# Kernel optimization log

Hardware: AMD Instinct MI355X
Metric: run time of the kernel (lower is better)

## Reference

```python
import jax, jax.numpy as jnp
import numpy as np
import math

NUM_HEADS = 16


def _alibi_slopes(num_heads: int):
    # geometric sequence for power-of-2 head counts (paper's scheme)
    def slopes_pow2(n):
        start = 2.0 ** (-(2.0 ** (-(math.log2(n) - 3))))
        return [start * (start ** i) for i in range(n)]
    if math.log2(num_heads).is_integer():
        return slopes_pow2(num_heads)
    c = 2 ** math.floor(math.log2(num_heads))
    extra = slopes_pow2(2 * c)[0::2][: num_heads - c]
    return slopes_pow2(c) + extra


def setup_inputs() -> dict:
    key = jax.random.key(0)
    kq, kk, kv = jax.random.split(key, 3)
    B, H, S, D = 2, NUM_HEADS, 2048, 64
    q = jax.random.normal(kq, (B, H, S, D), dtype=jnp.float32)
    k = jax.random.normal(kk, (B, H, S, D), dtype=jnp.float32)
    v = jax.random.normal(kv, (B, H, S, D), dtype=jnp.float32)
    return {"q": q, "k": k, "v": v}


def reference(q, k, v):
    B, H, Sq, D = q.shape
    Sk = k.shape[2]
    slopes = jnp.asarray(_alibi_slopes(H), dtype=jnp.float32)  # [H]
    pos = jnp.arange(Sk)
    # abs relative positions (symmetric, non-causal) as in the source
    rel = jnp.abs(pos[None, :] - pos[:, None]).astype(jnp.float32)  # [Sk, Sk]
    alibi = -slopes[:, None, None] * rel[None, :Sq, :]  # [H, Sq, Sk]
    scores = jnp.einsum("bhqd,bhkd->bhqk", q, k) / math.sqrt(D)
    scores = scores + alibi[None]
    probs = jax.nn.softmax(scores, axis=-1)
    return jnp.einsum("bhqk,bhkd->bhqd", probs, v)
```

## Files before the change

kernel.cpp:

```cpp
#include <hip/hip_runtime.h>
#include <hip/hip_bf16.h>
#include <math.h>

typedef __bf16 bf16;
typedef __attribute__((ext_vector_type(8))) bf16 bf16x8;
typedef __attribute__((ext_vector_type(2))) bf16 bf16x2;
typedef __attribute__((ext_vector_type(16))) float f32x16;
typedef __attribute__((ext_vector_type(4))) unsigned int uint4v;

#define SQ 2048
#define DH 64
#define NH 16
#define QBLK 128
#define KVT 64
#define NKVT (SQ / KVT)
#define LOG2E 1.44269504088896340736f

#define BUFSZ 16384
#define LDSV  8192

__device__ __forceinline__ int swz(int row, int colbyte) {
    return row * 128 + (colbyte ^ ((row & 7) << 4));
}

__device__ __forceinline__ float fast_exp2(float x) {
#if __has_builtin(__builtin_amdgcn_exp2f)
    return __builtin_amdgcn_exp2f(x);
#else
    return exp2f(x);
#endif
}

__device__ __forceinline__ unsigned pkbf16(float a, float b) {
    union { bf16x2 h; unsigned u; } x;
    x.h = (bf16x2){(bf16)a, (bf16)b};
    return x.u;
}

#if __has_builtin(__builtin_amdgcn_permlane32_swap)
__device__ __forceinline__ void plswap(unsigned &a, unsigned &b) {
    typedef __attribute__((ext_vector_type(2))) unsigned int uint2v;
    uint2v r = __builtin_amdgcn_permlane32_swap(a, b, false, false);
    a = r[0]; b = r[1];
}
#else
__device__ __forceinline__ void plswap(unsigned &a, unsigned &b) {
    asm volatile("v_permlane32_swap_b32 %0, %1" : "+v"(a), "+v"(b));
}
#endif

#if __has_builtin(__builtin_amdgcn_global_load_lds)
#define HAVE_GLL 1
__device__ __forceinline__ void async_copy16(const bf16* g, char* l) {
    __builtin_amdgcn_global_load_lds(
        (const __attribute__((address_space(1))) unsigned int*)g,
        (__attribute__((address_space(3))) unsigned int*)l, 16, 0, 0);
}
#else
#define HAVE_GLL 0
#endif

union FragU { uint4v u; bf16x8 b; };

__global__ __launch_bounds__(256)
void alibi_prep_kernel(const float* __restrict__ K, const float* __restrict__ V,
                       bf16* __restrict__ Kb, bf16* __restrict__ Vtb) {
    __shared__ bf16 lt[64][72];
    const int t  = threadIdx.x;
    const int s0 = blockIdx.x * 64;
    const int bh = blockIdx.y;
    if (blockIdx.z == 0) {
        const float* src = K + (size_t)bh * SQ * DH + (size_t)s0 * DH;
        bf16* dst = Kb + (size_t)bh * SQ * DH + (size_t)s0 * DH;
#pragma unroll
        for (int i = 0; i < 2; ++i) {
            int idx = t + 256 * i;
            int row = idx >> 3, c8 = idx & 7;
            const float* p = src + row * DH + c8 * 8;
            float4 a = *(const float4*)p, b = *(const float4*)(p + 4);
            bf16x8 pk = {(bf16)a.x,(bf16)a.y,(bf16)a.z,(bf16)a.w,
                         (bf16)b.x,(bf16)b.y,(bf16)b.z,(bf16)b.w};
            *(bf16x8*)(dst + row * DH + c8 * 8) = pk;
        }
    } else {
        const float* src = V + (size_t)bh * SQ * DH + (size_t)s0 * DH;
#pragma unroll
        for (int i = 0; i < 2; ++i) {
            int idx = t + 256 * i;
            int row = idx >> 3, c8 = idx & 7;
            const float* p = src + row * DH + c8 * 8;
            float4 a = *(const float4*)p, b = *(const float4*)(p + 4);
            bf16 e[8] = {(bf16)a.x,(bf16)a.y,(bf16)a.z,(bf16)a.w,
                         (bf16)b.x,(bf16)b.y,(bf16)b.z,(bf16)b.w};
#pragma unroll
            for (int j = 0; j < 8; ++j) lt[c8 * 8 + j][row] = e[j];
        }
        __syncthreads();
        bf16* dst = Vtb + (size_t)bh * DH * SQ;
#pragma unroll
        for (int i = 0; i < 2; ++i) {
            int idx = t + 256 * i;
            int d = idx >> 3, c8 = idx & 7;
            *(bf16x8*)(dst + (size_t)d * SQ + s0 + c8 * 8) = *(const bf16x8*)&lt[d][c8 * 8];
        }
    }
}

__global__ __launch_bounds__(256)
void alibi_attn_kernel(const float* __restrict__ Q, const bf16* __restrict__ Kb,
                       const bf16* __restrict__ Vtb, float* __restrict__ Out) {
    __shared__ __align__(16) char lds[3 * BUFSZ];
    const int tid  = threadIdx.x;
    const int lane = tid & 63;
    const int wave = tid >> 6;
    const int r32  = lane & 31;
    const int hi   = lane >> 5;
    const int l8   = lane >> 3;

    const int b   = blockIdx.x;
    const int r   = (b < 256) ? b : 767 - b;
    const int h   = 15 - (r >> 5);
    const int sub = r & 31;
    const int bh  = (sub >> 4) * NH + h;
    const int q0  = (sub & 15) * QBLK;

    const float slope2  = exp2f(-0.5f * (float)(h + 1)) * LOG2E;
    const float SLOPE2N = -slope2;
    const float QSCALE  = 0.125f * LOG2E;

    const int D = (int)(24.0f / slope2);
    const int a0 = q0 - D;
    const int tmin = (a0 <= 0) ? 0 : (a0 >> 6);
    const int tmax = min(NKVT - 1, (q0 + QBLK - 1 + D) >> 6);

    const size_t base = (size_t)bh * SQ * DH;
    const float* Qp = Q + base;
    const bf16*  Kp = Kb + base;
    const bf16*  Vp = Vtb + base;
    float*       Op = Out + base;

    const int qrow = q0 + wave * 32 + r32;
    bf16x8 qfrag[4];
#pragma unroll
    for (int dstep = 0; dstep < 4; ++dstep) {
        const float* sq = Qp + (size_t)qrow * DH + dstep * 16 + hi * 8;
        float4 a = *(const float4*)sq, bb = *(const float4*)(sq + 4);
        qfrag[dstep] = (bf16x8){(bf16)(a.x*QSCALE),(bf16)(a.y*QSCALE),
                                (bf16)(a.z*QSCALE),(bf16)(a.w*QSCALE),
                                (bf16)(bb.x*QSCALE),(bf16)(bb.y*QSCALE),
                                (bf16)(bb.z*QSCALE),(bf16)(bb.w*QSCALE)};
    }

    f32x16 oacc[2];
#pragma unroll
    for (int d = 0; d < 2; ++d)
#pragma unroll
        for (int rr = 0; rr < 16; ++rr) oacc[d][rr] = 0.f;
    float ps0 = 0.f, ps1 = 0.f, ps2 = 0.f, ps3 = 0.f;
    const float qh = (float)(qrow - 4 * hi);

    const int cswz = ((lane & 7) << 4) ^ ((l8 & 7) << 4);

    auto STAGE = [&](int bufi, int kvtile) {
        char* lb = lds + bufi * BUFSZ;
        const int kv0 = kvtile * KVT;
#pragma unroll
        for (int i = 0; i < 2; ++i) {
            const int chunk = wave * 2 + i;
            const int row = chunk * 8 + l8;
            const bf16* gK = Kp + (size_t)(kv0 + row) * DH + (cswz >> 1);
            const bf16* gV = Vp + (size_t)row * SQ + kv0 + (cswz >> 1);
#if HAVE_GLL
            async_copy16(gK, lb + chunk * 1024);
            async_copy16(gV, lb + LDSV + chunk * 1024);
#else
            *(bf16x8*)(lb + chunk * 1024 + lane * 16) = *(const bf16x8*)gK;
            *(bf16x8*)(lb + LDSV + chunk * 1024 + lane * 16) = *(const bf16x8*)gV;
#endif
        }
    };

    STAGE(0, tmin);
    STAGE(1, tmin + 1);
    asm volatile("s_waitcnt vmcnt(4)" ::: "memory");
    __builtin_amdgcn_s_barrier();
    __builtin_amdgcn_sched_barrier(0);

    int cb = 0, sb = 2;

    for (int t = tmin; t <= tmax; ++t) {
        const int kv0 = t * KVT;
        const char* lb = lds + cb * BUFSZ;

        f32x16 sacc[2];
        __builtin_amdgcn_s_setprio(1);
#pragma unroll
        for (int blk = 0; blk < 2; ++blk) {
            f32x16 acc;
#pragma unroll
            for (int rr = 0; rr < 16; ++rr) acc[rr] = 0.f;
#pragma unroll
            for (int dstep = 0; dstep < 4; ++dstep) {
                bf16x8 kf = *(const bf16x8*)(lb + swz(blk * 32 + r32, dstep * 32 + hi * 16));
                acc = __builtin_amdgcn_mfma_f32_32x32x16_bf16(kf, qfrag[dstep], acc, 0, 0, 0);
            }
            sacc[blk] = acc;
        }
        __builtin_amdgcn_s_setprio(0);

        STAGE(sb, min(t + 2, tmax));

        const float gq = qh - (float)kv0;
        float p[32];
#pragma unroll
        for (int blk = 0; blk < 2; ++blk)
#pragma unroll
            for (int reg = 0; reg < 16; ++reg) {
                const int krel = (reg & 3) + 8 * (reg >> 2) + 32 * blk;
                float d = gq - (float)krel;
                float s2 = fmaf(SLOPE2N, fabsf(d), sacc[blk][reg]);
                float e = fast_exp2(s2);
                p[blk * 16 + reg] = e;
                if ((reg & 3) == 0) ps0 += e;
                else if ((reg & 3) == 1) ps1 += e;
                else if ((reg & 3) == 2) ps2 += e;
                else ps3 += e;
            }

        __builtin_amdgcn_s_setprio(1);
#pragma unroll
        for (int kstep = 0; kstep < 4; ++kstep) {
            const int b16 = (kstep >> 1) * 16;
            const int R = (kstep & 1) * 8;
            unsigned w0 = pkbf16(p[b16 + R + 0], p[b16 + R + 1]);
            unsigned w1 = pkbf16(p[b16 + R + 2], p[b16 + R + 3]);
            unsigned w2 = pkbf16(p[b16 + R + 4], p[b16 + R + 5]);
            unsigned w3 = pkbf16(p[b16 + R + 6], p[b16 + R + 7]);
            plswap(w0, w2);
            plswap(w1, w3);
            FragU pf; pf.u = (uint4v){w0, w1, w2, w3};
#pragma unroll
            for (int dblk = 0; dblk < 2; ++dblk) {
                bf16x8 vf = *(const bf16x8*)(lb + LDSV + swz(dblk * 32 + r32, kstep * 32 + hi * 16));
                oacc[dblk] = __builtin_amdgcn_mfma_f32_32x32x16_bf16(vf, pf.b, oacc[dblk], 0, 0, 0);
            }
        }
        __builtin_amdgcn_s_setprio(0);

        asm volatile("s_waitcnt vmcnt(4)" ::: "memory");
        __builtin_amdgcn_s_barrier();
        __builtin_amdgcn_sched_barrier(0);

        cb = (cb == 2) ? 0 : cb + 1;
        sb = (sb == 2) ? 0 : sb + 1;
    }

    float psum = (ps0 + ps1) + (ps2 + ps3);
    psum += __shfl_xor(psum, 32);
    const float inv = 1.f / psum;
#pragma unroll
    for (int dblk = 0; dblk < 2; ++dblk)
#pragma unroll
        for (int g2 = 0; g2 < 4; ++g2) {
            float4 o = {oacc[dblk][4*g2+0] * inv, oacc[dblk][4*g2+1] * inv,
                        oacc[dblk][4*g2+2] * inv, oacc[dblk][4*g2+3] * inv};
            *(float4*)(Op + (size_t)qrow * DH + dblk * 32 + g2 * 8 + hi * 4) = o;
        }
}

extern "C" void kernel_launch(void* const* d_in, const int* in_sizes, int n_in,
                              void* d_out, int out_size, void* d_ws, size_t ws_size,
                              hipStream_t stream) {
    const float* q = (const float*)d_in[0];
    const float* k = (const float*)d_in[1];
    const float* v = (const float*)d_in[2];
    float* out = (float*)d_out;
    const int BH = in_sizes[0] / (SQ * DH);
    bf16* Kb  = (bf16*)d_ws;
    bf16* Vtb = (bf16*)((char*)d_ws + (size_t)BH * SQ * DH * sizeof(bf16));
    alibi_prep_kernel<<<dim3(SQ / 64, BH, 2), dim3(256), 0, stream>>>(k, v, Kb, Vtb);
    alibi_attn_kernel<<<dim3(512), dim3(256), 0, stream>>>(q, Kb, Vtb, out);
}
```

Before: 54.02 us.

## Split KV tiles across wave pairs with smaller Q blocks and LDS reduction

Q block size is halved to 64 rows, which doubles the grid to 1024 blocks. Inside each block the two wave pairs handle alternate KV tiles for the same 64 query rows, and their partial outputs and row sums are combined through LDS at the end. The triple-buffered async prefetch is replaced by a load, wait-all, compute loop, and launch bounds now ask for 4 blocks per CU. The aim is better occupancy and load balance across the alibi-banded work, at the cost of losing overlap between loads and compute and adding an epilogue reduction.

```diff
diff --git a/kernel.cpp b/kernel.cpp
--- a/kernel.cpp
+++ b/kernel.cpp
@@ -11,13 +11,14 @@
 #define SQ 2048
 #define DH 64
 #define NH 16
-#define QBLK 128
+#define QBLK 64
 #define KVT 64
 #define NKVT (SQ / KVT)
 #define LOG2E 1.44269504088896340736f
 
-#define BUFSZ 16384
+#define PBUF  16384
 #define LDSV  8192
+#define LDS_BYTES 32768
 
 __device__ __forceinline__ int swz(int row, int colbyte) {
     return row * 128 + (colbyte ^ ((row & 7) << 4));
@@ -106,23 +107,31 @@
     }
 }
 
-__global__ __launch_bounds__(256)
+__global__ __launch_bounds__(256, 4)
 void alibi_attn_kernel(const float* __restrict__ Q, const bf16* __restrict__ Kb,
                        const bf16* __restrict__ Vtb, float* __restrict__ Out) {
-    __shared__ __align__(16) char lds[3 * BUFSZ];
-    const int tid  = threadIdx.x;
-    const int lane = tid & 63;
-    const int wave = tid >> 6;
-    const int r32  = lane & 31;
-    const int hi   = lane >> 5;
-    const int l8   = lane >> 3;
-
-    const int b   = blockIdx.x;
-    const int r   = (b < 256) ? b : 767 - b;
-    const int h   = 15 - (r >> 5);
-    const int sub = r & 31;
-    const int bh  = (sub >> 4) * NH + h;
-    const int q0  = (sub & 15) * QBLK;
+    __shared__ __align__(16) char lds[LDS_BYTES];
+    const int tid   = threadIdx.x;
+    const int lane  = tid & 63;
+    const int wave  = tid >> 6;
+    const int par   = wave >> 1;
+    const int kind  = wave & 1;
+    const int qhalf = wave & 1;
+    const int r32   = lane & 31;
+    const int hi    = lane >> 5;
+    const int l8    = lane >> 3;
+
+    const int b  = blockIdx.x;
+    const int qd = b >> 8, i = b & 255;
+    int r;
+    if      (qd == 0) r = i;
+    else if (qd == 1) r = 511 - i;
+    else if (qd == 2) r = 512 + i;
+    else              r = 1023 - i;
+    const int h   = 15 - (r >> 6);
+    const int sub = r & 63;
+    const int bh  = (sub >> 5) * NH + h;
+    const int q0  = (sub & 31) * QBLK;
 
     const float slope2  = exp2f(-0.5f * (float)(h + 1)) * LOG2E;
     const float SLOPE2N = -slope2;
@@ -132,6 +141,7 @@
     const int a0 = q0 - D;
     const int tmin = (a0 <= 0) ? 0 : (a0 >> 6);
     const int tmax = min(NKVT - 1, (q0 + QBLK - 1 + D) >> 6);
+    const int nsteps = ((tmax - tmin + 1) + 1) >> 1;
 
     const size_t base = (size_t)bh * SQ * DH;
     const float* Qp = Q + base;
@@ -139,7 +149,7 @@
     const bf16*  Vp = Vtb + base;
     float*       Op = Out + base;
 
-    const int qrow = q0 + wave * 32 + r32;
+    const int qrow = q0 + qhalf * 32 + r32;
     bf16x8 qfrag[4];
 #pragma unroll
     for (int dstep = 0; dstep < 4; ++dstep) {
@@ -159,113 +169,142 @@
     float ps0 = 0.f, ps1 = 0.f, ps2 = 0.f, ps3 = 0.f;
     const float qh = (float)(qrow - 4 * hi);
 
-    const int cswz = ((lane & 7) << 4) ^ ((l8 & 7) << 4);
-
-    auto STAGE = [&](int bufi, int kvtile) {
-        char* lb = lds + bufi * BUFSZ;
-        const int kv0 = kvtile * KVT;
-#pragma unroll
-        for (int i = 0; i < 2; ++i) {
-            const int chunk = wave * 2 + i;
-            const int row = chunk * 8 + l8;
-            const bf16* gK = Kp + (size_t)(kv0 + row) * DH + (cswz >> 1);
-            const bf16* gV = Vp + (size_t)row * SQ + kv0 + (cswz >> 1);
+    const int cswz = ((lane & 7) << 4) ^ (l8 << 4);
+    char* const sbuf = lds + par * PBUF + kind * LDSV;
+    const char* const cbuf = lds + par * PBUF;
+
+    for (int s = 0; s < nsteps; ++s) {
+        const int tc = tmin + 2 * s + par;
+        const int ts = min(tc, tmax);
+
+        {
+            const int kv0s = ts * KVT;
+            if (kind == 0) {
+#pragma unroll
+                for (int c = 0; c < 8; ++c) {
+                    const int row = c * 8 + l8;
+                    const bf16* gK = Kp + (size_t)(kv0s + row) * DH + (cswz >> 1);
 #if HAVE_GLL
-            async_copy16(gK, lb + chunk * 1024);
-            async_copy16(gV, lb + LDSV + chunk * 1024);
-#else
-            *(bf16x8*)(lb + chunk * 1024 + lane * 16) = *(const bf16x8*)gK;
-            *(bf16x8*)(lb + LDSV + chunk * 1024 + lane * 16) = *(const bf16x8*)gV;
-#endif
-        }
-    };
-
-    STAGE(0, tmin);
-    STAGE(1, tmin + 1);
-    asm volatile("s_waitcnt vmcnt(4)" ::: "memory");
-    __builtin_amdgcn_s_barrier();
-    __builtin_amdgcn_sched_barrier(0);
-
-    int cb = 0, sb = 2;
-
-    for (int t = tmin; t <= tmax; ++t) {
-        const int kv0 = t * KVT;
-        const char* lb = lds + cb * BUFSZ;
-
-        f32x16 sacc[2];
-        __builtin_amdgcn_s_setprio(1);
-#pragma unroll
-        for (int blk = 0; blk < 2; ++blk) {
-            f32x16 acc;
-#pragma unroll
-            for (int rr = 0; rr < 16; ++rr) acc[rr] = 0.f;
-#pragma unroll
-            for (int dstep = 0; dstep < 4; ++dstep) {
-                bf16x8 kf = *(const bf16x8*)(lb + swz(blk * 32 + r32, dstep * 32 + hi * 16));
-                acc = __builtin_amdgcn_mfma_f32_32x32x16_bf16(kf, qfrag[dstep], acc, 0, 0, 0);
-            }
-            sacc[blk] = acc;
-        }
-        __builtin_amdgcn_s_setprio(0);
-
-        STAGE(sb, min(t + 2, tmax));
-
-        const float gq = qh - (float)kv0;
-        float p[32];
-#pragma unroll
-        for (int blk = 0; blk < 2; ++blk)
-#pragma unroll
-            for (int reg = 0; reg < 16; ++reg) {
-                const int krel = (reg & 3) + 8 * (reg >> 2) + 32 * blk;
-                float d = gq - (float)krel;
-                float s2 = fmaf(SLOPE2N, fabsf(d), sacc[blk][reg]);
-                float e = fast_exp2(s2);
-                p[blk * 16 + reg] = e;
-                if ((reg & 3) == 0) ps0 += e;
-                else if ((reg & 3) == 1) ps1 += e;
-                else if ((reg & 3) == 2) ps2 += e;
-                else ps3 += e;
-            }
-
-        __builtin_amdgcn_s_setprio(1);
-#pragma unroll
-        for (int kstep = 0; kstep < 4; ++kstep) {
-            const int b16 = (kstep >> 1) * 16;
-            const int R = (kstep & 1) * 8;
-            unsigned w0 = pkbf16(p[b16 + R + 0], p[b16 + R + 1]);
-            unsigned w1 = pkbf16(p[b16 + R + 2], p[b16 + R + 3]);
-            unsigned w2 = pkbf16(p[b16 + R + 4], p[b16 + R + 5]);
-            unsigned w3 = pkbf16(p[b16 + R + 6], p[b16 + R + 7]);
-            plswap(w0, w2);
-            plswap(w1, w3);
-            FragU pf; pf.u = (uint4v){w0, w1, w2, w3};
-#pragma unroll
-            for (int dblk = 0; dblk < 2; ++dblk) {
-                bf16x8 vf = *(const bf16x8*)(lb + LDSV + swz(dblk * 32 + r32, kstep * 32 + hi * 16));
-                oacc[dblk] = __builtin_amdgcn_mfma_f32_32x32x16_bf16(vf, pf.b, oacc[dblk], 0, 0, 0);
-            }
-        }
-        __builtin_amdgcn_s_setprio(0);
-
-        asm volatile("s_waitcnt vmcnt(4)" ::: "memory");
+                    async_copy16(gK, sbuf + c * 1024);
+#else
+                    *(bf16x8*)(sbuf + c * 1024 + lane * 16) = *(const bf16x8*)gK;
+#endif
+                }
+            } else {
+#pragma unroll
+                for (int c = 0; c < 8; ++c) {
+                    const int row = c * 8 + l8;
+                    const bf16* gV = Vp + (size_t)row * SQ + kv0s + (cswz >> 1);
+#if HAVE_GLL
+                    async_copy16(gV, sbuf + c * 1024);
+#else
+                    *(bf16x8*)(sbuf + c * 1024 + lane * 16) = *(const bf16x8*)gV;
+#endif
+                }
+            }
+        }
+        asm volatile("s_waitcnt vmcnt(0)" ::: "memory");
         __builtin_amdgcn_s_barrier();
         __builtin_amdgcn_sched_barrier(0);
 
-        cb = (cb == 2) ? 0 : cb + 1;
-        sb = (sb == 2) ? 0 : sb + 1;
+        if (tc <= tmax) {
+            const int kv0 = tc * KVT;
+
+            f32x16 sacc[2];
+            __builtin_amdgcn_s_setprio(1);
+#pragma unroll
+            for (int blk = 0; blk < 2; ++blk) {
+                f32x16 acc;
+#pragma unroll
+                for (int rr = 0; rr < 16; ++rr) acc[rr] = 0.f;
+#pragma unroll
+                for (int dstep = 0; dstep < 4; ++dstep) {
+                    bf16x8 kf = *(const bf16x8*)(cbuf + swz(blk * 32 + r32, dstep * 32 + hi * 16));
+                    acc = __builtin_amdgcn_mfma_f32_32x32x16_bf16(kf, qfrag[dstep], acc, 0, 0, 0);
+                }
+                sacc[blk] = acc;
+            }
+            __builtin_amdgcn_s_setprio(0);
+
+            const float gq = qh - (float)kv0;
+            float p[32];
+#pragma unroll
+            for (int blk = 0; blk < 2; ++blk)
+#pragma unroll
+                for (int reg = 0; reg < 16; ++reg) {
+                    const int krel = (reg & 3) + 8 * (reg >> 2) + 32 * blk;
+                    float d = gq - (float)krel;
+                    float s2 = fmaf(SLOPE2N, fabsf(d), sacc[blk][reg]);
+                    float e = fast_exp2(s2);
+                    p[blk * 16 + reg] = e;
+                    if ((reg & 3) == 0) ps0 += e;
+                    else if ((reg & 3) == 1) ps1 += e;
+                    else if ((reg & 3) == 2) ps2 += e;
+                    else ps3 += e;
+                }
+
+            __builtin_amdgcn_s_setprio(1);
+#pragma unroll
+            for (int kstep = 0; kstep < 4; ++kstep) {
+                const int b16 = (kstep >> 1) * 16;
+                const int R = (kstep & 1) * 8;
+                unsigned w0 = pkbf16(p[b16 + R + 0], p[b16 + R + 1]);
+                unsigned w1 = pkbf16(p[b16 + R + 2], p[b16 + R + 3]);
+                unsigned w2 = pkbf16(p[b16 + R + 4], p[b16 + R + 5]);
+                unsigned w3 = pkbf16(p[b16 + R + 6], p[b16 + R + 7]);
+                plswap(w0, w2);
+                plswap(w1, w3);
+                FragU pf; pf.u = (uint4v){w0, w1, w2, w3};
+#pragma unroll
+                for (int dblk = 0; dblk < 2; ++dblk) {
+                    bf16x8 vf = *(const bf16x8*)(cbuf + LDSV + swz(dblk * 32 + r32, kstep * 32 + hi * 16));
+                    oacc[dblk] = __builtin_amdgcn_mfma_f32_32x32x16_bf16(vf, pf.b, oacc[dblk], 0, 0, 0);
+                }
+            }
+            __builtin_amdgcn_s_setprio(0);
+        }
+        __builtin_amdgcn_s_barrier();
+        __builtin_amdgcn_sched_barrier(0);
     }
 
     float psum = (ps0 + ps1) + (ps2 + ps3);
     psum += __shfl_xor(psum, 32);
-    const float inv = 1.f / psum;
-#pragma unroll
-    for (int dblk = 0; dblk < 2; ++dblk)
-#pragma unroll
-        for (int g2 = 0; g2 < 4; ++g2) {
-            float4 o = {oacc[dblk][4*g2+0] * inv, oacc[dblk][4*g2+1] * inv,
-                        oacc[dblk][4*g2+2] * inv, oacc[dblk][4*g2+3] * inv};
-            *(float4*)(Op + (size_t)qrow * DH + dblk * 32 + g2 * 8 + hi * 4) = o;
-        }
+
+    __syncthreads();
+    float* ep = (float*)lds + qhalf * (64 * 36);
+    float* slot = ep + lane * 36;
+    if (par == 1) {
+#pragma unroll
+        for (int dblk = 0; dblk < 2; ++dblk)
+#pragma unroll
+            for (int g2 = 0; g2 < 4; ++g2)
+                *(float4*)(slot + dblk * 16 + g2 * 4) =
+                    (float4){oacc[dblk][4*g2+0], oacc[dblk][4*g2+1],
+                             oacc[dblk][4*g2+2], oacc[dblk][4*g2+3]};
+        slot[32] = psum;
+    }
+    __syncthreads();
+    if (par == 0) {
+#pragma unroll
+        for (int dblk = 0; dblk < 2; ++dblk)
+#pragma unroll
+            for (int g2 = 0; g2 < 4; ++g2) {
+                float4 o = *(const float4*)(slot + dblk * 16 + g2 * 4);
+                oacc[dblk][4*g2+0] += o.x; oacc[dblk][4*g2+1] += o.y;
+                oacc[dblk][4*g2+2] += o.z; oacc[dblk][4*g2+3] += o.w;
+            }
+        psum += slot[32];
+
+        const float inv = 1.f / psum;
+#pragma unroll
+        for (int dblk = 0; dblk < 2; ++dblk)
+#pragma unroll
+            for (int g2 = 0; g2 < 4; ++g2) {
+                float4 o = {oacc[dblk][4*g2+0] * inv, oacc[dblk][4*g2+1] * inv,
+                            oacc[dblk][4*g2+2] * inv, oacc[dblk][4*g2+3] * inv};
+                *(float4*)(Op + (size_t)qrow * DH + dblk * 32 + g2 * 8 + hi * 4) = o;
+            }
+    }
 }
 
 extern "C" void kernel_launch(void* const* d_in, const int* in_sizes, int n_in,
@@ -279,5 +318,6 @@
     bf16* Kb  = (bf16*)d_ws;
     bf16* Vtb = (bf16*)((char*)d_ws + (size_t)BH * SQ * DH * sizeof(bf16));
     alibi_prep_kernel<<<dim3(SQ / 64, BH, 2), dim3(256), 0, stream>>>(k, v, Kb, Vtb);
-    alibi_attn_kernel<<<dim3(512), dim3(256), 0, stream>>>(q, Kb, Vtb, out);
-}
+    const int nblk = BH * (SQ / QBLK);
+    alibi_attn_kernel<<<dim3(nblk), dim3(256), 0, stream>>>(q, Kb, Vtb, out);
+}
```

Result: faster. 49.67 us (-8.1%).
